# Kernel tuning notes

Measured on AMD Instinct MI355X. Metric: run time of the kernel, lower is better.

## Reference

```python
import jax, jax.numpy as jnp
import numpy as np
from jax import lax

N = 32768      # total nodes (8 graphs x 4096)
E = 262144     # edges (avg degree 8)
B = 8          # graphs in batch
TW = 25        # time window
H = 128        # hidden features
L = 6          # GNN layers
NV = 1         # n_variables (pos_t only)
SD = 1         # spatial dim
TMAX, TMIN, RES_T = 4.0, 0.0, 250.0
BD_LOW, BD_UP = 0.0, 16.0
EPS = 1e-5


def swish(x):
    return x * jax.nn.sigmoid(x)


def setup_inputs() -> dict:
    key = jax.random.key(0)
    ks = jax.random.split(key, 32)
    s = 0.05
    u = jax.random.normal(ks[0], (N, TW), jnp.float32)
    pos_t = jax.random.uniform(ks[1], (N, 1), jnp.float32) * TMAX
    pos_x = jax.random.uniform(ks[2], (N, 1), jnp.float32) * BD_UP
    pos = jnp.concatenate([pos_t, pos_x], axis=-1)
    edge_index = jax.random.randint(ks[3], (2, E), 0, N, jnp.int64)
    batch = jnp.repeat(jnp.arange(B, dtype=jnp.int64), N // B)
    d_in = TW + SD + NV          # 27
    d_msg = 2 * H + TW + SD + NV  # 282
    d_upd = H + H + NV            # 257
    We1 = jax.random.normal(ks[4], (d_in, H), jnp.float32) * s
    be1 = jnp.zeros((H,), jnp.float32)
    We2 = jax.random.normal(ks[5], (H, H), jnp.float32) * s
    be2 = jnp.zeros((H,), jnp.float32)
    Wm1 = jax.random.normal(ks[6], (L, d_msg, H), jnp.float32) * s
    bm1 = jnp.zeros((L, H), jnp.float32)
    Wm2 = jax.random.normal(ks[7], (L, H, H), jnp.float32) * s
    bm2 = jnp.zeros((L, H), jnp.float32)
    Wu1 = jax.random.normal(ks[8], (L, d_upd, H), jnp.float32) * s
    bu1 = jnp.zeros((L, H), jnp.float32)
    Wu2 = jax.random.normal(ks[9], (L, H, H), jnp.float32) * s
    bu2 = jnp.zeros((L, H), jnp.float32)
    Wc1 = jax.random.normal(ks[10], (8, 1, 16), jnp.float32) * s  # OIH
    bc1 = jnp.zeros((8,), jnp.float32)
    Wc2 = jax.random.normal(ks[11], (1, 8, 14), jnp.float32) * s
    bc2 = jnp.zeros((1,), jnp.float32)
    return dict(u=u, pos=pos, edge_index=edge_index, batch=batch,
                We1=We1, be1=be1, We2=We2, be2=be2,
                Wm1=Wm1, bm1=bm1, Wm2=Wm2, bm2=bm2,
                Wu1=Wu1, bu1=bu1, Wu2=Wu2, bu2=bu2,
                Wc1=Wc1, bc1=bc1, Wc2=Wc2, bc2=bc2)


def _mpnn(u, pos, edge_index, batch, We1, be1, We2, be2,
          Wm1, bm1, Wm2, bm2, Wu1, bu1, Wu2, bu2, Wc1, bc1, Wc2, bc2):
    src = edge_index[0]   # j (source)
    tgt = edge_index[1]   # i (target)
    pos_t = pos[:, 0:1] / TMAX
    pos_x = (pos[:, 1:] - BD_LOW) / (BD_UP - BD_LOW)
    variables = pos_t  # eq_variables empty -> only normalized time

    node_input = jnp.concatenate([u, pos_x, variables], axis=-1)  # [N, 27]
    h = swish(node_input @ We1 + be1)
    h = swish(h @ We2 + be2)

    # in-degree for scatter-mean (empty targets -> 0 like PyG mean)
    cnt = jnp.zeros((N,), jnp.float32).at[tgt].add(1.0)
    cnt = jnp.maximum(cnt, 1.0)[:, None]
    # per-graph node counts for InstanceNorm
    gcnt = jax.ops.segment_sum(jnp.ones((N,), jnp.float32), batch, num_segments=B)[:, None]

    u_diff_e = u[tgt] - u[src]          # [E, TW]
    p_diff_e = pos_x[tgt] - pos_x[src]  # [E, SD]
    var_i_e = variables[tgt]            # [E, NV]

    for l in range(L):
        # message: gather -> MLP per edge
        m_in = jnp.concatenate([h[tgt], h[src], u_diff_e, p_diff_e, var_i_e], axis=-1)  # [E, 282]
        msg = swish(m_in @ Wm1[l] + bm1[l])
        msg = swish(msg @ Wm2[l] + bm2[l])
        # scatter-mean aggregate onto targets
        agg = jax.ops.segment_sum(msg, tgt, num_segments=N) / cnt  # [N, H]
        # node update MLP, residual (in_features == out_features)
        up = jnp.concatenate([h, agg, variables], axis=-1)  # [N, 257]
        up = swish(up @ Wu1[l] + bu1[l])
        up = swish(up @ Wu2[l] + bu2[l])
        h = h + up
        # InstanceNorm per graph (no affine), biased variance
        mean = jax.ops.segment_sum(h, batch, num_segments=B) / gcnt      # [B, H]
        sq = jax.ops.segment_sum(h * h, batch, num_segments=B) / gcnt    # [B, H]
        var = sq - mean * mean
        h = (h - mean[batch]) / jnp.sqrt(var[batch] + EPS)

    # output CNN: tw=25 branch
    hc = h[:, None, :]  # [N, 1, 128]
    dn = ('NCH', 'OIH', 'NCH')
    c = lax.conv_general_dilated(hc, Wc1, (3,), 'VALID', dimension_numbers=dn) + bc1[None, :, None]
    c = swish(c)
    c = lax.conv_general_dilated(c, Wc2, (1,), 'VALID', dimension_numbers=dn) + bc2[None, :, None]
    diff = c[:, 0, :]  # [N, 25]

    dt = (TMAX - TMIN) / RES_T
    dt_cum = jnp.arange(1, TW + 1, dtype=jnp.float32) * dt  # cumsum of ones*dt
    out = u[:, -1:] + dt_cum[None, :] * diff
    return out


def reference(u, pos, edge_index, batch, We1, be1, We2, be2,
              Wm1, bm1, Wm2, bm2, Wu1, bu1, Wu2, bu2, Wc1, bc1, Wc2, bc2):
    return _mpnn(u, pos, edge_index, batch, We1, be1, We2, be2,
                 Wm1, bm1, Wm2, bm2, Wu1, bu1, Wu2, bu2, Wc1, bc1, Wc2, bc2)
```

## Files before the change

kernel.cpp:

```cpp
#include <hip/hip_runtime.h>
#include <stdint.h>

#define N_NODES 32768
#define N_EDGES 262144
#define NB 8
#define TW 25

typedef __attribute__((ext_vector_type(8))) short short8;
typedef __attribute__((ext_vector_type(4))) float floatx4;

#if defined(__has_builtin)
#if __has_builtin(__builtin_amdgcn_cvt_pk_bf16_f32)
#define HAVE_CVT_PK_BF16 1
#endif
#endif

__device__ __forceinline__ float swishf(float x) {
    return x * __builtin_amdgcn_rcpf(1.0f + __expf(-x));
}

__device__ __forceinline__ unsigned short f2bf(float x) {
    union { float f; unsigned u; } v; v.f = x;
    unsigned r = v.u + 0x7FFFu + ((v.u >> 16) & 1u);
    return (unsigned short)(r >> 16);
}
__device__ __forceinline__ unsigned pkbf(float a, float b) {
#ifdef HAVE_CVT_PK_BF16
    typedef __attribute__((ext_vector_type(2))) __bf16 bf16x2;
    union { bf16x2 v; unsigned u; } cv;
    cv.v = __builtin_amdgcn_cvt_pk_bf16_f32(a, b);
    return cv.u;
#else
    return (unsigned)f2bf(a) | ((unsigned)f2bf(b) << 16);
#endif
}
__device__ __forceinline__ float bf2f(unsigned short b) {
    union { unsigned u; float f; } v; v.u = ((unsigned)b) << 16; return v.f;
}

__global__ void init_kernel(const float* __restrict__ pos,
                            float* __restrict__ posx, float* __restrict__ post) {
    int i = blockIdx.x * 256 + threadIdx.x;
    if (i < N_NODES) {
        post[i] = pos[i * 2 + 0] * 0.25f;
        posx[i] = pos[i * 2 + 1] * 0.0625f;
    }
}

__global__ void deg_kernel(const int* __restrict__ tgt, int* __restrict__ deg) {
    int i = blockIdx.x * 256 + threadIdx.x;
    if (i < N_EDGES) atomicAdd(&deg[tgt[i]], 1);
}

__global__ __launch_bounds__(1024) void scan_kernel(const int* __restrict__ deg,
                                                    int* __restrict__ cursor) {
    __shared__ int ps[1024];
    int t = threadIdx.x;
    int base = t * 32;
    int tot = 0;
    for (int i = 0; i < 32; ++i) tot += deg[base + i];
    ps[t] = tot;
    __syncthreads();
    for (int off = 1; off < 1024; off <<= 1) {
        int v = (t >= off) ? ps[t - off] : 0;
        __syncthreads();
        ps[t] += v;
        __syncthreads();
    }
    int run = ps[t] - tot;
    for (int i = 0; i < 32; ++i) {
        cursor[base + i] = run;
        run += deg[base + i];
    }
}

__global__ void scatter_kernel(const int* __restrict__ src, const int* __restrict__ tgt,
                               int* __restrict__ cursor,
                               int* __restrict__ src_s, int* __restrict__ tgt_s) {
    int i = blockIdx.x * 256 + threadIdx.x;
    if (i < N_EDGES) {
        int tg = tgt[i];
        int p = atomicAdd(&cursor[tg], 1);
        src_s[p] = src[i];
        tgt_s[p] = tg;
    }
}

__global__ __launch_bounds__(256) void ediff_kernel(
    const float* __restrict__ u, const float* __restrict__ posx,
    const float* __restrict__ post,
    const int* __restrict__ src_s, const int* __restrict__ tgt_s,
    unsigned short* __restrict__ ediff)
{
    int e = blockIdx.x * 256 + threadIdx.x;
    if (e >= N_EDGES) return;
    int s = src_s[e], g = tgt_s[e];
    float fv[32];
    #pragma unroll
    for (int k = 0; k < 32; ++k) fv[k] = 0.f;
    #pragma unroll
    for (int k = 0; k < 25; ++k)
        fv[k] = u[(size_t)g * 25 + k] - u[(size_t)s * 25 + k];
    fv[25] = posx[g] - posx[s];
    fv[26] = post[g];
    unsigned pk[16];
    #pragma unroll
    for (int j = 0; j < 16; ++j) pk[j] = pkbf(fv[2 * j], fv[2 * j + 1]);
    #pragma unroll
    for (int j = 0; j < 4; ++j)
        *(uint4*)(ediff + (size_t)e * 32 + j * 8) = *(uint4*)&pk[j * 4];
}

__global__ __launch_bounds__(256) void pack_kernel(const float* __restrict__ W,
                                                   unsigned short* __restrict__ Wp,
                                                   int Kreal, int Kc, int total) {
    int id = blockIdx.x * 256 + threadIdx.x;
    if (id >= total) return;
    int lane = id & 63;
    int t8 = (id >> 6) & 7;
    int rest = id >> 9;
    int c = rest % Kc;
    int l = rest / Kc;
    int n = t8 * 16 + (lane & 15);
    int kb = c * 32 + (lane >> 4) * 8;
    short8 v;
    #pragma unroll
    for (int j = 0; j < 8; ++j) {
        int k = kb + j;
        float x = (k < Kreal) ? W[((size_t)l * Kreal + k) * 128 + n] : 0.f;
        v[j] = (short)f2bf(x);
    }
    *(short8*)(Wp + (size_t)id * 8) = v;
}

__global__ __launch_bounds__(256) void encoder_kernel(
    const float* __restrict__ u, const float* __restrict__ posx,
    const float* __restrict__ post,
    const float* __restrict__ We1, const float* __restrict__ be1,
    const float* __restrict__ We2, const float* __restrict__ be2,
    float* __restrict__ h, unsigned short* __restrict__ h_bf,
    float* __restrict__ agg)
{
    __shared__ __align__(16) float As[64 * 36];
    __shared__ __align__(16) float Ws[32 * 128];
    __shared__ __align__(16) float Ms[64 * 128];

    int t = threadIdx.x;
    int n0 = blockIdx.x * 64;
    int rg = t >> 5, cg = t & 31;

    {
        int r = t & 63, cseg = t >> 6;
        float4 z = make_float4(0.f, 0.f, 0.f, 0.f);
        #pragma unroll
        for (int j = 0; j < 8; ++j)
            *(float4*)(agg + (size_t)(n0 + r) * 128 + cseg * 32 + j * 4) = z;
    }

    float acc[8][4] = {};
    {
        int kk = t >> 3, cb = (t & 7) * 16;
        #pragma unroll
        for (int j = 0; j < 4; ++j) {
            float4 w = make_float4(0.f, 0.f, 0.f, 0.f);
            if (kk < 27) w = *(const float4*)&We1[kk * 128 + cb + j * 4];
            *(float4*)&Ws[kk * 128 + cb + j * 4] = w;
        }
        int el = t >> 2, kb = (t & 3) * 8, n = n0 + el;
        float v[8];
        #pragma unroll
        for (int j = 0; j < 8; ++j) {
            int k = kb + j;
            float x = 0.f;
            if (k < 25) x = u[n * 25 + k];
            else if (k == 25) x = posx[n];
            else if (k == 26) x = post[n];
            v[j] = x;
        }
        #pragma unroll
        for (int j = 0; j < 8; j += 4)
            *(float4*)&As[el * 36 + kb + j] = make_float4(v[j], v[j+1], v[j+2], v[j+3]);
        __syncthreads();
        #pragma unroll 4
        for (int kk2 = 0; kk2 < 32; ++kk2) {
            float4 b = *(const float4*)&Ws[kk2 * 128 + cg * 4];
            float a[8];
            #pragma unroll
            for (int i = 0; i < 8; ++i) a[i] = As[(rg * 8 + i) * 36 + kk2];
            #pragma unroll
            for (int i = 0; i < 8; ++i) {
                acc[i][0] += a[i] * b.x; acc[i][1] += a[i] * b.y;
                acc[i][2] += a[i] * b.z; acc[i][3] += a[i] * b.w;
            }
        }
        __syncthreads();
    }
    {
        float4 b1 = *(const float4*)&be1[cg * 4];
        #pragma unroll
        for (int i = 0; i < 8; ++i) {
            float4 m;
            m.x = swishf(acc[i][0] + b1.x);
            m.y = swishf(acc[i][1] + b1.y);
            m.z = swishf(acc[i][2] + b1.z);
            m.w = swishf(acc[i][3] + b1.w);
            *(float4*)&Ms[(rg * 8 + i) * 128 + cg * 4] = m;
        }
        __syncthreads();
    }
    float acc2[8][4] = {};
    for (int k0 = 0; k0 < 128; k0 += 32) {
        int kk = t >> 3, cb = (t & 7) * 16;
        #pragma unroll
        for (int j = 0; j < 4; ++j)
            *(float4*)&Ws[kk * 128 + cb + j * 4] =
                *(const float4*)&We2[(k0 + kk) * 128 + cb + j * 4];
        __syncthreads();
        #pragma unroll 4
        for (int kk2 = 0; kk2 < 32; ++kk2) {
            float4 b = *(const float4*)&Ws[kk2 * 128 + cg * 4];
            float a[8];
            #pragma unroll
            for (int i = 0; i < 8; ++i) a[i] = Ms[(rg * 8 + i) * 128 + (k0 + kk2)];
            #pragma unroll
            for (int i = 0; i < 8; ++i) {
                acc2[i][0] += a[i] * b.x; acc2[i][1] += a[i] * b.y;
                acc2[i][2] += a[i] * b.z; acc2[i][3] += a[i] * b.w;
            }
        }
        __syncthreads();
    }
    {
        float4 b2 = *(const float4*)&be2[cg * 4];
        #pragma unroll
        for (int i = 0; i < 8; ++i) {
            int n = n0 + rg * 8 + i;
            float4 o;
            o.x = swishf(acc2[i][0] + b2.x);
            o.y = swishf(acc2[i][1] + b2.y);
            o.z = swishf(acc2[i][2] + b2.z);
            o.w = swishf(acc2[i][3] + b2.w);
            *(float4*)&h[(size_t)n * 128 + cg * 4] = o;
            uint2 pk;
            pk.x = pkbf(o.x, o.y);
            pk.y = pkbf(o.z, o.w);
            *(uint2*)(h_bf + (size_t)n * 128 + cg * 4) = pk;
        }
    }
}

__global__ __launch_bounds__(512, 8) void message_kernel(
    const unsigned short* __restrict__ h_bf,
    const unsigned short* __restrict__ ediff,
    const int* __restrict__ src_s, const int* __restrict__ tgt_s,
    const unsigned short* __restrict__ W1p, const float* __restrict__ b1,
    const unsigned short* __restrict__ W2p, const float* __restrict__ b2,
    float* __restrict__ agg, float* __restrict__ stats)
{
    __shared__ __align__(16) unsigned short SH[64 * 296];
    __shared__ int tgtS[64];
    unsigned short* Msh = SH;
    unsigned short* Cs  = SH + 9216;

    int t = threadIdx.x;
    int e0 = blockIdx.x * 64;
    if (blockIdx.x == 0 && t < 256) {
        float4 z = make_float4(0.f, 0.f, 0.f, 0.f);
        *(float4*)&stats[t * 8] = z;
        *(float4*)&stats[t * 8 + 4] = z;
    }
    if (t < 64) tgtS[t] = tgt_s[e0 + t];

    {
        int r = t & 63, cseg = t >> 6;
        int g = tgt_s[e0 + r], s = src_s[e0 + r];
        const short8* hg = (const short8*)(h_bf + (size_t)g * 128);
        const short8* hs = (const short8*)(h_bf + (size_t)s * 128);
        #pragma unroll
        for (int j = 0; j < 2; ++j) {
            int chunk = cseg * 2 + j;
            *(short8*)(SH + r * 296 + chunk * 8)       = hg[chunk];
            *(short8*)(SH + r * 296 + 128 + chunk * 8) = hs[chunk];
        }
        if (cseg < 4)
            *(short8*)(SH + r * 296 + 256 + cseg * 8) =
                *(const short8*)(ediff + (size_t)(e0 + r) * 32 + cseg * 8);
    }
    __syncthreads();

    int w = t >> 6, lane = t & 63, q = lane >> 4, m = lane & 15;

    floatx4 acc[4] = {};
    #pragma unroll
    for (int c = 0; c < 9; ++c) {
        short8 b = *(const short8*)(W1p + ((size_t)(c * 8 + w) * 64 + lane) * 8);
        #pragma unroll
        for (int g2 = 0; g2 < 4; ++g2) {
            short8 a = *(const short8*)(SH + (g2 * 16 + m) * 296 + c * 32 + q * 8);
            acc[g2] = __builtin_amdgcn_mfma_f32_16x16x32_bf16(a, b, acc[g2], 0, 0, 0);
        }
    }
    __syncthreads();

    {
        int col = w * 16 + m;
        float bv = b1[col];
        #pragma unroll
        for (int g2 = 0; g2 < 4; ++g2) {
            unsigned p01 = pkbf(swishf(acc[g2][0] + bv), swishf(acc[g2][1] + bv));
            unsigned p23 = pkbf(swishf(acc[g2][2] + bv), swishf(acc[g2][3] + bv));
            int base = g2 * 16 + q * 4;
            Msh[(base + 0) * 136 + col] = (unsigned short)p01;
            Msh[(base + 1) * 136 + col] = (unsigned short)(p01 >> 16);
            Msh[(base + 2) * 136 + col] = (unsigned short)p23;
            Msh[(base + 3) * 136 + col] = (unsigned short)(p23 >> 16);
        }
    }
    __syncthreads();

    floatx4 acc2[4] = {};
    #pragma unroll
    for (int c = 0; c < 4; ++c) {
        short8 b = *(const short8*)(W2p + ((size_t)(c * 8 + w) * 64 + lane) * 8);
        #pragma unroll
        for (int g2 = 0; g2 < 4; ++g2) {
            short8 a = *(const short8*)(Msh + (g2 * 16 + m) * 136 + c * 32 + q * 8);
            acc2[g2] = __builtin_amdgcn_mfma_f32_16x16x32_bf16(a, b, acc2[g2], 0, 0, 0);
        }
    }
    {
        int col = w * 16 + m;
        float bv = b2[col];
        #pragma unroll
        for (int g2 = 0; g2 < 4; ++g2) {
            unsigned p01 = pkbf(swishf(acc2[g2][0] + bv), swishf(acc2[g2][1] + bv));
            unsigned p23 = pkbf(swishf(acc2[g2][2] + bv), swishf(acc2[g2][3] + bv));
            int base = g2 * 16 + q * 4;
            Cs[(base + 0) * 132 + col] = (unsigned short)p01;
            Cs[(base + 1) * 132 + col] = (unsigned short)(p01 >> 16);
            Cs[(base + 2) * 132 + col] = (unsigned short)p23;
            Cs[(base + 3) * 132 + col] = (unsigned short)(p23 >> 16);
        }
    }
    __syncthreads();

    {
        int col = t & 127, seg = t >> 7;
        int r0 = seg * 16;
        float run = 0.f;
        int prev = tgtS[r0];
        bool atStart = true;
        #pragma unroll 4
        for (int i = 0; i < 16; ++i) {
            int tg = tgtS[r0 + i];
            if (tg != prev) {
                float* dst = &agg[(size_t)prev * 128 + col];
                if (atStart) atomicAdd(dst, run);
                else *dst = run;
                run = 0.f; prev = tg; atStart = false;
            }
            run += bf2f(Cs[(r0 + i) * 132 + col]);
        }
        atomicAdd(&agg[(size_t)prev * 128 + col], run);
    }
}

__global__ __launch_bounds__(512, 4) void update_kernel(
    float* __restrict__ h, const unsigned short* __restrict__ h_bf,
    float* __restrict__ agg, const int* __restrict__ deg,
    const float* __restrict__ post,
    const unsigned short* __restrict__ W1p, const float* __restrict__ b1,
    const unsigned short* __restrict__ W2p, const float* __restrict__ b2,
    float* __restrict__ stats)
{
    __shared__ __align__(16) unsigned short SH[64 * 296];
    unsigned short* Msh = SH;

    int t = threadIdx.x;
    int n0 = blockIdx.x * 64;

    {
        int r = t & 63, cseg = t >> 6;
        int n = n0 + r;
        const short8* hn = (const short8*)(h_bf + (size_t)n * 128);
        #pragma unroll
        for (int j = 0; j < 2; ++j) {
            int chunk = cseg * 2 + j;
            *(short8*)(SH + r * 296 + chunk * 8) = hn[chunk];
        }
        float ic = __builtin_amdgcn_rcpf(fmaxf((float)deg[n], 1.0f));
        #pragma unroll
        for (int j = 0; j < 2; ++j) {
            int unit = cseg * 2 + j;
            const float* ap = agg + (size_t)n * 128 + unit * 8;
            float4 v0 = *(const float4*)ap;
            float4 v1 = *(const float4*)(ap + 4);
            unsigned pa[4];
            pa[0] = pkbf(v0.x * ic, v0.y * ic);
            pa[1] = pkbf(v0.z * ic, v0.w * ic);
            pa[2] = pkbf(v1.x * ic, v1.y * ic);
            pa[3] = pkbf(v1.z * ic, v1.w * ic);
            *(uint4*)(SH + r * 296 + 128 + unit * 8) = *(uint4*)pa;
        }
        if (cseg < 4) {
            short8 z;
            #pragma unroll
            for (int k = 0; k < 8; ++k) z[k] = 0;
            if (cseg == 0) z[0] = (short)f2bf(post[n]);
            *(short8*)(SH + r * 296 + 256 + cseg * 8) = z;
        }
    }
    __syncthreads();

    int w = t >> 6, lane = t & 63, q = lane >> 4, m = lane & 15;

    floatx4 acc[4] = {};
    #pragma unroll
    for (int c = 0; c < 9; ++c) {
        short8 b = *(const short8*)(W1p + ((size_t)(c * 8 + w) * 64 + lane) * 8);
        #pragma unroll
        for (int g2 = 0; g2 < 4; ++g2) {
            short8 a = *(const short8*)(SH + (g2 * 16 + m) * 296 + c * 32 + q * 8);
            acc[g2] = __builtin_amdgcn_mfma_f32_16x16x32_bf16(a, b, acc[g2], 0, 0, 0);
        }
    }
    __syncthreads();

    {
        int col = w * 16 + m;
        float bv = b1[col];
        #pragma unroll
        for (int g2 = 0; g2 < 4; ++g2) {
            unsigned p01 = pkbf(swishf(acc[g2][0] + bv), swishf(acc[g2][1] + bv));
            unsigned p23 = pkbf(swishf(acc[g2][2] + bv), swishf(acc[g2][3] + bv));
            int base = g2 * 16 + q * 4;
            Msh[(base + 0) * 136 + col] = (unsigned short)p01;
            Msh[(base + 1) * 136 + col] = (unsigned short)(p01 >> 16);
            Msh[(base + 2) * 136 + col] = (unsigned short)p23;
            Msh[(base + 3) * 136 + col] = (unsigned short)(p23 >> 16);
        }
    }
    __syncthreads();

    floatx4 acc2[4] = {};
    #pragma unroll
    for (int c = 0; c < 4; ++c) {
        short8 b = *(const short8*)(W2p + ((size_t)(c * 8 + w) * 64 + lane) * 8);
        #pragma unroll
        for (int g2 = 0; g2 < 4; ++g2) {
            short8 a = *(const short8*)(Msh + (g2 * 16 + m) * 136 + c * 32 + q * 8);
            acc2[g2] = __builtin_amdgcn_mfma_f32_16x16x32_bf16(a, b, acc2[g2], 0, 0, 0);
        }
    }

    int bidx = n0 >> 12;
    int col = w * 16 + m;
    float bv = b2[col];
    float s = 0.f, s2 = 0.f;
    #pragma unroll
    for (int g2 = 0; g2 < 4; ++g2) {
        #pragma unroll
        for (int r = 0; r < 4; ++r) {
            int row = g2 * 16 + q * 4 + r;
            size_t i0 = (size_t)(n0 + row) * 128 + col;
            float hv = h[i0] + swishf(acc2[g2][r] + bv);
            h[i0] = hv;
            s += hv; s2 += hv * hv;
        }
    }
    s  += __shfl_xor(s, 16);  s  += __shfl_xor(s, 32);
    s2 += __shfl_xor(s2, 16); s2 += __shfl_xor(s2, 32);
    if (q == 0) {
        atomicAdd(&stats[bidx * 128 + col], s);
        atomicAdd(&stats[(NB + bidx) * 128 + col], s2);
    }
    {
        int r = t & 63, cseg = t >> 6;
        float4 z = make_float4(0.f, 0.f, 0.f, 0.f);
        #pragma unroll
        for (int j = 0; j < 4; ++j)
            *(float4*)(agg + (size_t)(n0 + r) * 128 + cseg * 16 + j * 4) = z;
    }
}

__global__ __launch_bounds__(256) void norm_kernel(float* __restrict__ h,
                                                   unsigned short* __restrict__ h_bf,
                                                   const float* __restrict__ stats) {
    size_t id = (size_t)blockIdx.x * 256 + threadIdx.x;
    int n = (int)(id >> 5), c4 = (int)(id & 31) * 4;
    int b = n >> 12;
    float4 mn = *(const float4*)&stats[b * 128 + c4];
    float4 sq = *(const float4*)&stats[(NB + b) * 128 + c4];
    float4 v = *(const float4*)&h[(size_t)n * 128 + c4];
    float4 r;
    float m0 = mn.x * (1.f / 4096.f), m1 = mn.y * (1.f / 4096.f);
    float m2 = mn.z * (1.f / 4096.f), m3 = mn.w * (1.f / 4096.f);
    r.x = (v.x - m0) * rsqrtf(sq.x * (1.f / 4096.f) - m0 * m0 + 1e-5f);
    r.y = (v.y - m1) * rsqrtf(sq.y * (1.f / 4096.f) - m1 * m1 + 1e-5f);
    r.z = (v.z - m2) * rsqrtf(sq.z * (1.f / 4096.f) - m2 * m2 + 1e-5f);
    r.w = (v.w - m3) * rsqrtf(sq.w * (1.f / 4096.f) - m3 * m3 + 1e-5f);
    *(float4*)&h[(size_t)n * 128 + c4] = r;
    uint2 pk;
    pk.x = pkbf(r.x, r.y);
    pk.y = pkbf(r.z, r.w);
    *(uint2*)(h_bf + (size_t)n * 128 + c4) = pk;
}

__global__ __launch_bounds__(256) void conv_kernel(
    const float* __restrict__ h, const float* __restrict__ u,
    const float* __restrict__ Wc1, const float* __restrict__ bc1,
    const float* __restrict__ Wc2, const float* __restrict__ bc2,
    float* __restrict__ out)
{
    __shared__ float hs[4][128];
    __shared__ float c1[4][8 * 40];
    int w = threadIdx.x >> 6, lane = threadIdx.x & 63;
    int n = blockIdx.x * 4 + w;
    hs[w][lane] = h[(size_t)n * 128 + lane];
    hs[w][lane + 64] = h[(size_t)n * 128 + lane + 64];
    __syncthreads();
    for (int idx = lane; idx < 304; idx += 64) {
        int o = idx / 38, p = idx % 38;
        float s = bc1[o];
        #pragma unroll
        for (int k = 0; k < 16; ++k) s += hs[w][p * 3 + k] * Wc1[o * 16 + k];
        c1[w][o * 40 + p] = swishf(s);
    }
    __syncthreads();
    if (lane < TW) {
        float s = bc2[0];
        #pragma unroll
        for (int o = 0; o < 8; ++o)
            for (int k = 0; k < 14; ++k)
                s += c1[w][o * 40 + lane + k] * Wc2[o * 14 + k];
        float dt_cum = (float)(lane + 1) * (4.0f / 250.0f);
        out[n * TW + lane] = u[n * 25 + 24] + dt_cum * s;
    }
}

extern "C" void kernel_launch(void* const* d_in, const int* in_sizes, int n_in,
                              void* d_out, int out_size, void* d_ws, size_t ws_size,
                              hipStream_t stream)
{
    const float* u   = (const float*)d_in[0];
    const float* pos = (const float*)d_in[1];
    const int*   ei  = (const int*)d_in[2];
    const float* We1 = (const float*)d_in[4];
    const float* be1 = (const float*)d_in[5];
    const float* We2 = (const float*)d_in[6];
    const float* be2 = (const float*)d_in[7];
    const float* Wm1 = (const float*)d_in[8];
    const float* bm1 = (const float*)d_in[9];
    const float* Wm2 = (const float*)d_in[10];
    const float* bm2 = (const float*)d_in[11];
    const float* Wu1 = (const float*)d_in[12];
    const float* bu1 = (const float*)d_in[13];
    const float* Wu2 = (const float*)d_in[14];
    const float* bu2 = (const float*)d_in[15];
    const float* Wc1 = (const float*)d_in[16];
    const float* bc1 = (const float*)d_in[17];
    const float* Wc2 = (const float*)d_in[18];
    const float* bc2 = (const float*)d_in[19];
    float* out = (float*)d_out;

    char* base = (char*)d_ws;
    size_t off = 0;
    auto alloc = [&](size_t bytes) -> char* {
        char* r = base + off;
        off = (off + bytes + 511) & ~(size_t)511;
        return r;
    };
    float*          h      = (float*)alloc((size_t)N_NODES * 128 * 4);
    unsigned short* h_bf   = (unsigned short*)alloc((size_t)N_NODES * 128 * 2);
    float*          agg    = (float*)alloc((size_t)N_NODES * 128 * 4);
    float*          posx   = (float*)alloc(N_NODES * 4);
    float*          post   = (float*)alloc(N_NODES * 4);
    float*          stats  = (float*)alloc(2 * NB * 128 * 4);
    int*            deg    = (int*)alloc(N_NODES * 4);
    int*            cursor = (int*)alloc(N_NODES * 4);
    int*            src_s  = (int*)alloc((size_t)N_EDGES * 4);
    int*            tgt_s  = (int*)alloc((size_t)N_EDGES * 4);
    unsigned short* ediff  = (unsigned short*)alloc((size_t)N_EDGES * 32 * 2);
    unsigned short* Wm1p   = (unsigned short*)alloc((size_t)6 * 9 * 4096 * 2);
    unsigned short* Wm2p   = (unsigned short*)alloc((size_t)6 * 4 * 4096 * 2);
    unsigned short* Wu1p   = (unsigned short*)alloc((size_t)6 * 9 * 4096 * 2);
    unsigned short* Wu2p   = (unsigned short*)alloc((size_t)6 * 4 * 4096 * 2);
    (void)ws_size;

    const int* srcp = ei;
    const int* tgtp = ei + N_EDGES;

    init_kernel<<<N_NODES / 256, 256, 0, stream>>>(pos, posx, post);
    hipMemsetAsync(deg, 0, N_NODES * sizeof(int), stream);
    deg_kernel<<<N_EDGES / 256, 256, 0, stream>>>(tgtp, deg);
    scan_kernel<<<1, 1024, 0, stream>>>(deg, cursor);
    scatter_kernel<<<N_EDGES / 256, 256, 0, stream>>>(srcp, tgtp, cursor, src_s, tgt_s);
    ediff_kernel<<<N_EDGES / 256, 256, 0, stream>>>(u, posx, post, src_s, tgt_s, ediff);
    encoder_kernel<<<N_NODES / 64, 256, 0, stream>>>(u, posx, post, We1, be1, We2, be2,
                                                     h, h_bf, agg);
    {
        int tot1 = 6 * 9 * 512;
        int tot2 = 6 * 4 * 512;
        pack_kernel<<<(tot1 + 255) / 256, 256, 0, stream>>>(Wm1, Wm1p, 283, 9, tot1);
        pack_kernel<<<(tot2 + 255) / 256, 256, 0, stream>>>(Wm2, Wm2p, 128, 4, tot2);
        pack_kernel<<<(tot1 + 255) / 256, 256, 0, stream>>>(Wu1, Wu1p, 257, 9, tot1);
        pack_kernel<<<(tot2 + 255) / 256, 256, 0, stream>>>(Wu2, Wu2p, 128, 4, tot2);
    }

    for (int l = 0; l < 6; ++l) {
        message_kernel<<<N_EDGES / 64, 512, 0, stream>>>(
            h_bf, ediff, src_s, tgt_s,
            Wm1p + (size_t)l * 9 * 4096, bm1 + l * 128,
            Wm2p + (size_t)l * 4 * 4096, bm2 + l * 128, agg, stats);
        update_kernel<<<N_NODES / 64, 512, 0, stream>>>(
            h, h_bf, agg, deg, post,
            Wu1p + (size_t)l * 9 * 4096, bu1 + l * 128,
            Wu2p + (size_t)l * 4 * 4096, bu2 + l * 128, stats);
        norm_kernel<<<(N_NODES * 32) / 256, 256, 0, stream>>>(h, h_bf, stats);
    }

    conv_kernel<<<N_NODES / 4, 256, 0, stream>>>(h, u, Wc1, bc1, Wc2, bc2, out);
}
```

Baseline: 692.0 us.

## Drop fp32 hidden state; keep residual stream in bf16 throughout

Removes the fp32 copy of the node features. The update kernel takes its residual from the bf16 h tile already staged in shared memory and writes the pre-norm value as bf16. The norm and conv kernels now read bf16. Separate LDS regions for the input tile and the intermediate also remove one barrier. This cuts global traffic per layer, at the cost of rounding the residual to bf16 at every layer, which may change accuracy.

```diff
diff --git a/kernel.cpp b/kernel.cpp
--- a/kernel.cpp
+++ b/kernel.cpp
@@ -138,8 +138,7 @@
     const float* __restrict__ post,
     const float* __restrict__ We1, const float* __restrict__ be1,
     const float* __restrict__ We2, const float* __restrict__ be2,
-    float* __restrict__ h, unsigned short* __restrict__ h_bf,
-    float* __restrict__ agg)
+    unsigned short* __restrict__ h_bf, float* __restrict__ agg)
 {
     __shared__ __align__(16) float As[64 * 36];
     __shared__ __align__(16) float Ws[32 * 128];
@@ -240,7 +239,6 @@
             o.y = swishf(acc2[i][1] + b2.y);
             o.z = swishf(acc2[i][2] + b2.z);
             o.w = swishf(acc2[i][3] + b2.w);
-            *(float4*)&h[(size_t)n * 128 + cg * 4] = o;
             uint2 pk;
             pk.x = pkbf(o.x, o.y);
             pk.y = pkbf(o.z, o.w);
@@ -366,15 +364,15 @@
 }
 
 __global__ __launch_bounds__(512, 4) void update_kernel(
-    float* __restrict__ h, const unsigned short* __restrict__ h_bf,
+    unsigned short* __restrict__ hraw, const unsigned short* __restrict__ h_bf,
     float* __restrict__ agg, const int* __restrict__ deg,
     const float* __restrict__ post,
     const unsigned short* __restrict__ W1p, const float* __restrict__ b1,
     const unsigned short* __restrict__ W2p, const float* __restrict__ b2,
     float* __restrict__ stats)
 {
-    __shared__ __align__(16) unsigned short SH[64 * 296];
-    unsigned short* Msh = SH;
+    __shared__ __align__(16) unsigned short SH[64 * 296 + 64 * 136];
+    unsigned short* Msh = SH + 64 * 296;
 
     int t = threadIdx.x;
     int n0 = blockIdx.x * 64;
@@ -424,8 +422,6 @@
             acc[g2] = __builtin_amdgcn_mfma_f32_16x16x32_bf16(a, b, acc[g2], 0, 0, 0);
         }
     }
-    __syncthreads();
-
     {
         int col = w * 16 + m;
         float bv = b1[col];
@@ -462,9 +458,9 @@
         #pragma unroll
         for (int r = 0; r < 4; ++r) {
             int row = g2 * 16 + q * 4 + r;
-            size_t i0 = (size_t)(n0 + row) * 128 + col;
-            float hv = h[i0] + swishf(acc2[g2][r] + bv);
-            h[i0] = hv;
+            float res = bf2f(SH[row * 296 + col]);
+            float hv = res + swishf(acc2[g2][r] + bv);
+            hraw[(size_t)(n0 + row) * 128 + col] = f2bf(hv);
             s += hv; s2 += hv * hv;
         }
     }
@@ -483,31 +479,35 @@
     }
 }
 
-__global__ __launch_bounds__(256) void norm_kernel(float* __restrict__ h,
-                                                   unsigned short* __restrict__ h_bf,
-                                                   const float* __restrict__ stats) {
+__global__ __launch_bounds__(256) void norm_kernel(
+    const unsigned short* __restrict__ hraw,
+    unsigned short* __restrict__ h_bf,
+    const float* __restrict__ stats)
+{
     size_t id = (size_t)blockIdx.x * 256 + threadIdx.x;
     int n = (int)(id >> 5), c4 = (int)(id & 31) * 4;
     int b = n >> 12;
     float4 mn = *(const float4*)&stats[b * 128 + c4];
     float4 sq = *(const float4*)&stats[(NB + b) * 128 + c4];
-    float4 v = *(const float4*)&h[(size_t)n * 128 + c4];
-    float4 r;
+    uint2 rawp = *(const uint2*)(hraw + (size_t)n * 128 + c4);
+    float v0 = bf2f((unsigned short)(rawp.x & 0xffffu));
+    float v1 = bf2f((unsigned short)(rawp.x >> 16));
+    float v2 = bf2f((unsigned short)(rawp.y & 0xffffu));
+    float v3 = bf2f((unsigned short)(rawp.y >> 16));
     float m0 = mn.x * (1.f / 4096.f), m1 = mn.y * (1.f / 4096.f);
     float m2 = mn.z * (1.f / 4096.f), m3 = mn.w * (1.f / 4096.f);
-    r.x = (v.x - m0) * rsqrtf(sq.x * (1.f / 4096.f) - m0 * m0 + 1e-5f);
-    r.y = (v.y - m1) * rsqrtf(sq.y * (1.f / 4096.f) - m1 * m1 + 1e-5f);
-    r.z = (v.z - m2) * rsqrtf(sq.z * (1.f / 4096.f) - m2 * m2 + 1e-5f);
-    r.w = (v.w - m3) * rsqrtf(sq.w * (1.f / 4096.f) - m3 * m3 + 1e-5f);
-    *(float4*)&h[(size_t)n * 128 + c4] = r;
+    float r0 = (v0 - m0) * rsqrtf(sq.x * (1.f / 4096.f) - m0 * m0 + 1e-5f);
+    float r1 = (v1 - m1) * rsqrtf(sq.y * (1.f / 4096.f) - m1 * m1 + 1e-5f);
+    float r2 = (v2 - m2) * rsqrtf(sq.z * (1.f / 4096.f) - m2 * m2 + 1e-5f);
+    float r3 = (v3 - m3) * rsqrtf(sq.w * (1.f / 4096.f) - m3 * m3 + 1e-5f);
     uint2 pk;
-    pk.x = pkbf(r.x, r.y);
-    pk.y = pkbf(r.z, r.w);
+    pk.x = pkbf(r0, r1);
+    pk.y = pkbf(r2, r3);
     *(uint2*)(h_bf + (size_t)n * 128 + c4) = pk;
 }
 
 __global__ __launch_bounds__(256) void conv_kernel(
-    const float* __restrict__ h, const float* __restrict__ u,
+    const unsigned short* __restrict__ h_bf, const float* __restrict__ u,
     const float* __restrict__ Wc1, const float* __restrict__ bc1,
     const float* __restrict__ Wc2, const float* __restrict__ bc2,
     float* __restrict__ out)
@@ -516,8 +516,8 @@
     __shared__ float c1[4][8 * 40];
     int w = threadIdx.x >> 6, lane = threadIdx.x & 63;
     int n = blockIdx.x * 4 + w;
-    hs[w][lane] = h[(size_t)n * 128 + lane];
-    hs[w][lane + 64] = h[(size_t)n * 128 + lane + 64];
+    hs[w][lane]      = bf2f(h_bf[(size_t)n * 128 + lane]);
+    hs[w][lane + 64] = bf2f(h_bf[(size_t)n * 128 + lane + 64]);
     __syncthreads();
     for (int idx = lane; idx < 304; idx += 64) {
         int o = idx / 38, p = idx % 38;
@@ -570,7 +570,7 @@
         off = (off + bytes + 511) & ~(size_t)511;
         return r;
     };
-    float*          h      = (float*)alloc((size_t)N_NODES * 128 * 4);
+    unsigned short* hraw   = (unsigned short*)alloc((size_t)N_NODES * 128 * 2);
     unsigned short* h_bf   = (unsigned short*)alloc((size_t)N_NODES * 128 * 2);
     float*          agg    = (float*)alloc((size_t)N_NODES * 128 * 4);
     float*          posx   = (float*)alloc(N_NODES * 4);
@@ -597,7 +597,7 @@
     scatter_kernel<<<N_EDGES / 256, 256, 0, stream>>>(srcp, tgtp, cursor, src_s, tgt_s);
     ediff_kernel<<<N_EDGES / 256, 256, 0, stream>>>(u, posx, post, src_s, tgt_s, ediff);
     encoder_kernel<<<N_NODES / 64, 256, 0, stream>>>(u, posx, post, We1, be1, We2, be2,
-                                                     h, h_bf, agg);
+                                                     h_bf, agg);
     {
         int tot1 = 6 * 9 * 512;
         int tot2 = 6 * 4 * 512;
@@ -613,11 +613,11 @@
             Wm1p + (size_t)l * 9 * 4096, bm1 + l * 128,
             Wm2p + (size_t)l * 4 * 4096, bm2 + l * 128, agg, stats);
         update_kernel<<<N_NODES / 64, 512, 0, stream>>>(
-            h, h_bf, agg, deg, post,
+            hraw, h_bf, agg, deg, post,
             Wu1p + (size_t)l * 9 * 4096, bu1 + l * 128,
             Wu2p + (size_t)l * 4 * 4096, bu2 + l * 128, stats);
-        norm_kernel<<<(N_NODES * 32) / 256, 256, 0, stream>>>(h, h_bf, stats);
-    }
-
-    conv_kernel<<<N_NODES / 4, 256, 0, stream>>>(h, u, Wc1, bc1, Wc2, bc2, out);
-}
+        norm_kernel<<<(N_NODES * 32) / 256, 256, 0, stream>>>(hraw, h_bf, stats);
+    }
+
+    conv_kernel<<<N_NODES / 4, 256, 0, stream>>>(h_bf, u, Wc1, bc1, Wc2, bc2, out);
+}
```

Result: faster. 663.2 us, median of 2 (-4.2%).
